# Performance work log

Hardware: AMD Instinct MI355X
Metric: run time of the kernel (lower is better)

## Reference

```python
import jax, jax.numpy as jnp
import numpy as np

QMAX = 127.0
QMIN = -128.0


def setup_inputs() -> dict:
    key = jax.random.key(0)
    k1, k2, k3 = jax.random.split(key, 3)
    B, N, D, O = 4, 4096, 2048, 2048
    x = jax.random.normal(k1, (B, N, D), dtype=jnp.float32)
    weight = jax.random.normal(k2, (O, D), dtype=jnp.float32)
    bias = jax.random.normal(k3, (O,), dtype=jnp.float32)
    return {"x": x, "weight": weight, "bias": bias}


def reference(x, weight, bias):
    # --- per-row symmetric int8 quantization of the weight [O, D] ---
    w_max = jnp.clip(jnp.max(jnp.abs(weight), axis=1, keepdims=True), 1e-8, None)
    w_scale = (w_max / QMAX)                     # [O, 1]
    w_q = jnp.clip(jnp.round(weight / w_scale), QMIN, QMAX).astype(jnp.int8)
    w_scale = w_scale.squeeze(1).astype(jnp.float32)  # [O]

    # --- dynamic per-row symmetric int8 quantization of x [B, N, D] ---
    x_max = jnp.max(jnp.abs(x), axis=2, keepdims=True)       # [B, N, 1]
    x_scale = jnp.maximum(x_max / QMAX, 1e-12)               # [B, N, 1]
    x_q = jnp.clip(jnp.round(x / x_scale), QMIN, QMAX).astype(jnp.int8)

    # --- int8 GEMM accumulated in int32: [B,N,D] x [O,D]^T -> [B,N,O] ---
    acc = jnp.einsum("bnd,od->bno", x_q.astype(jnp.int32), w_q.astype(jnp.int32))

    # --- dequantize with per-row activation scale and per-out-channel weight scale ---
    y = acc.astype(jnp.float32) * x_scale.astype(jnp.float32) * w_scale[None, None, :]
    y = y + bias
    return y.astype(x.dtype)
```

## Files before the change

kernel.cpp:

```cpp
#include <hip/hip_runtime.h>
#include <stdint.h>
#include <stddef.h>

typedef int v4i __attribute__((ext_vector_type(4)));

#define GLOAD_LDS16(g, l) __builtin_amdgcn_global_load_lds( \
    (const __attribute__((address_space(1))) void*)(g),     \
    (__attribute__((address_space(3))) void*)(l), 16, 0, 0)

__device__ __forceinline__ int pack4(float4 f, float s) {
    int a = (int)rintf(f.x / s); a = a < -128 ? -128 : (a > 127 ? 127 : a);
    int b = (int)rintf(f.y / s); b = b < -128 ? -128 : (b > 127 ? 127 : b);
    int c = (int)rintf(f.z / s); c = c < -128 ? -128 : (c > 127 ? 127 : c);
    int d = (int)rintf(f.w / s); d = d < -128 ? -128 : (d > 127 ? 127 : d);
    return (a & 255) | ((b & 255) << 8) | ((c & 255) << 16) | ((d & 255) << 24);
}

__global__ __launch_bounds__(256) void quant_rows_2048(
    const float* __restrict__ in, signed char* __restrict__ q,
    float* __restrict__ scales, float floorv)
{
    const int lane = threadIdx.x & 63;
    const int row  = blockIdx.x * 4 + (threadIdx.x >> 6);
    const float* rp = in + (size_t)row * 2048;

    float4 v[8];
#pragma unroll
    for (int j = 0; j < 2; ++j) {
        const float4* p = (const float4*)(rp + j * 1024 + lane * 16);
#pragma unroll
        for (int i = 0; i < 4; ++i) v[j * 4 + i] = p[i];
    }
    float am = 0.0f;
#pragma unroll
    for (int i = 0; i < 8; ++i) {
        am = fmaxf(am, fabsf(v[i].x));
        am = fmaxf(am, fabsf(v[i].y));
        am = fmaxf(am, fabsf(v[i].z));
        am = fmaxf(am, fabsf(v[i].w));
    }
#pragma unroll
    for (int off = 32; off; off >>= 1) am = fmaxf(am, __shfl_xor(am, off));
    const float s = fmaxf(am / 127.0f, floorv);

#pragma unroll
    for (int j = 0; j < 2; ++j) {
        int4 pk;
        pk.x = pack4(v[j * 4 + 0], s);
        pk.y = pack4(v[j * 4 + 1], s);
        pk.z = pack4(v[j * 4 + 2], s);
        pk.w = pack4(v[j * 4 + 3], s);
        *(int4*)(q + (size_t)row * 2048 + j * 1024 + lane * 16) = pk;
    }
    if (lane == 0) scales[row] = s;
}

__global__ __launch_bounds__(512, 2) void gemm_i8_pipe(
    const signed char* __restrict__ xq, const signed char* __restrict__ wq,
    const float* __restrict__ xs, const float* __restrict__ ws,
    const float* __restrict__ bias, float* __restrict__ out, int K)
{
    __shared__ __align__(16) signed char lds[131072];

    const int tid  = threadIdx.x;
    const int lane = tid & 63;
    const int wid  = tid >> 6;
    const int wm   = wid >> 2;
    const int wn   = wid & 3;

    const int nwg  = gridDim.x * gridDim.y;
    int orig = blockIdx.y * gridDim.x + blockIdx.x;
    int swz  = ((nwg & 7) == 0) ? ((orig & 7) * (nwg >> 3) + (orig >> 3)) : orig;
    const int brow = (swz / gridDim.x) * 256;
    const int bcol = (swz % gridDim.x) * 256;

    const int srow = tid >> 2;
    const int gch  = (((tid & 3) ^ ((tid >> 3) & 3)) << 4);
    const int lofs = tid << 4;
    const signed char* gA = xq + (size_t)(brow + srow) * K;
    const signed char* gB = wq + (size_t)(bcol + srow) * K;

#define ST_A(tt, half) GLOAD_LDS16(gA + (size_t)(half) * 128 * K + (size_t)(tt) * 64 + gch, \
                                   lds + ((((tt) & 3) << 14) + ((half) << 13) + lofs))
#define ST_B(tt, half) GLOAD_LDS16(gB + (size_t)(half) * 128 * K + (size_t)(tt) * 64 + gch, \
                                   lds + (65536 + (((tt) & 3) << 14) + ((half) << 13) + lofs))

    const int rl   = lane & 15;
    const int ko   = lane >> 4;
    const int slot = ((ko ^ ((rl >> 1) & 3)) << 4);

#define FRAG_A(buf, r) (*(const v4i*)(lds + (((buf) << 14) + (r) * 64 + slot)))
#define FRAG_B(buf, r) (*(const v4i*)(lds + (65536 + ((buf) << 14) + (r) * 64 + slot)))

    v4i acc[8][4] = {};

#define MFMA8(M0, M1)                                                              \
    do {                                                                           \
        __builtin_amdgcn_s_setprio(1);                                             \
        acc[M0][0] = __builtin_amdgcn_mfma_i32_16x16x64_i8(a0, bf0, acc[M0][0], 0, 0, 0); \
        acc[M0][1] = __builtin_amdgcn_mfma_i32_16x16x64_i8(a0, bf1, acc[M0][1], 0, 0, 0); \
        acc[M0][2] = __builtin_amdgcn_mfma_i32_16x16x64_i8(a0, bf2, acc[M0][2], 0, 0, 0); \
        acc[M0][3] = __builtin_amdgcn_mfma_i32_16x16x64_i8(a0, bf3, acc[M0][3], 0, 0, 0); \
        acc[M1][0] = __builtin_amdgcn_mfma_i32_16x16x64_i8(a1, bf0, acc[M1][0], 0, 0, 0); \
        acc[M1][1] = __builtin_amdgcn_mfma_i32_16x16x64_i8(a1, bf1, acc[M1][1], 0, 0, 0); \
        acc[M1][2] = __builtin_amdgcn_mfma_i32_16x16x64_i8(a1, bf2, acc[M1][2], 0, 0, 0); \
        acc[M1][3] = __builtin_amdgcn_mfma_i32_16x16x64_i8(a1, bf3, acc[M1][3], 0, 0, 0); \
        __builtin_amdgcn_s_setprio(0);                                             \
    } while (0)

#define BAR()  __builtin_amdgcn_s_barrier()
#define LGKM0() asm volatile("s_waitcnt lgkmcnt(0)" ::: "memory")

    auto tile = [&](int t, bool issue) {
        const int buf = t & 3;
        const int ar  = wm * 128 + rl;
        const int br  = wn * 64 + rl;
        v4i bf0 = FRAG_B(buf, br);
        v4i bf1 = FRAG_B(buf, br + 16);
        v4i bf2 = FRAG_B(buf, br + 32);
        v4i bf3 = FRAG_B(buf, br + 48);
        v4i a0  = FRAG_A(buf, ar);
        v4i a1  = FRAG_A(buf, ar + 16);
        if (issue) ST_A(t + 3, 0);
        BAR(); LGKM0();
        MFMA8(0, 1);
        BAR();
        a0 = FRAG_A(buf, ar + 32);
        a1 = FRAG_A(buf, ar + 48);
        if (issue) ST_A(t + 3, 1);
        BAR(); LGKM0();
        MFMA8(2, 3);
        BAR();
        a0 = FRAG_A(buf, ar + 64);
        a1 = FRAG_A(buf, ar + 80);
        if (issue) ST_B(t + 3, 0);
        BAR(); LGKM0();
        MFMA8(4, 5);
        BAR();
        a0 = FRAG_A(buf, ar + 96);
        a1 = FRAG_A(buf, ar + 112);
        if (issue) ST_B(t + 3, 1);
        BAR(); LGKM0();
        MFMA8(6, 7);
    };

    ST_A(0, 0); ST_A(0, 1); ST_B(0, 0); ST_B(0, 1);
    ST_A(1, 0); ST_A(1, 1); ST_B(1, 0); ST_B(1, 1);
    ST_A(2, 0); ST_A(2, 1); ST_B(2, 0); ST_B(2, 1);
    asm volatile("s_waitcnt vmcnt(8)" ::: "memory");
    BAR();

    const int NT = K >> 6;
    int t = 0;
    for (; t < NT - 3; ++t) {
        tile(t, true);
        asm volatile("s_waitcnt vmcnt(8)" ::: "memory");
        BAR();
    }
    tile(NT - 3, false);
    asm volatile("s_waitcnt vmcnt(4)" ::: "memory");
    BAR();
    tile(NT - 2, false);
    asm volatile("s_waitcnt vmcnt(0)" ::: "memory");
    BAR();
    tile(NT - 1, false);

    const int rg = lane >> 4;
#pragma unroll
    for (int n = 0; n < 4; ++n) {
        const int col = bcol + wn * 64 + n * 16 + rl;
        const float wsc = ws[col];
        const float bv  = bias[col];
#pragma unroll
        for (int m = 0; m < 8; ++m) {
#pragma unroll
            for (int j = 0; j < 4; ++j) {
                const int row = brow + wm * 128 + m * 16 + rg * 4 + j;
                out[(size_t)row * 2048 + col] =
                    (float)acc[m][n][j] * xs[row] * wsc + bv;
            }
        }
    }
#undef ST_A
#undef ST_B
#undef FRAG_A
#undef FRAG_B
#undef MFMA8
#undef BAR
#undef LGKM0
}

extern "C" void kernel_launch(void* const* d_in, const int* in_sizes, int n_in,
                              void* d_out, int out_size, void* d_ws, size_t ws_size,
                              hipStream_t stream) {
    const float* x    = (const float*)d_in[0];
    const float* w    = (const float*)d_in[1];
    const float* bias = (const float*)d_in[2];
    float* out = (float*)d_out;

    const int D = 2048;
    const int O = in_sizes[2];
    const int M = in_sizes[0] / D;

    char* wsb = (char*)d_ws;
    signed char* xq  = (signed char*)wsb;
    signed char* wqp = (signed char*)(wsb + (size_t)M * D);
    float* xs  = (float*)(wsb + (size_t)M * D + (size_t)O * D);
    float* wsc = (float*)(wsb + (size_t)M * D + (size_t)O * D + (size_t)M * 4);

    quant_rows_2048<<<M / 4, 256, 0, stream>>>(x, xq, xs, 1e-12f);
    quant_rows_2048<<<O / 4, 256, 0, stream>>>(w, wqp, wsc, 1e-8f / 127.0f);

    dim3 grid(O / 256, M / 256);
    gemm_i8_pipe<<<grid, 512, 0, stream>>>(xq, wqp, xs, wsc, bias, out, D);
}
```

Measured before the change: 126.0 us.

## Software-pipeline LDS fragment reads one phase ahead of MFMA in GEMM loop

Restructures the main GEMM loop so the A and B LDS fragment reads for the next phase (and the next tile's B fragments) are issued before the current MFMA group. It waits only with lgkmcnt(3) instead of draining all LDS reads, which is meant to hide LDS latency behind matrix-core work. The per-tile lambda and its peeled tail are replaced by a single loop with conditional stores and vmcnt waits. This adds register pressure from the double-buffered fragments and relies on the lgkmcnt counting matching the order in which global-to-LDS loads and LDS reads are issued. A wrong count could read stale data.

```diff
diff --git a/kernel.cpp b/kernel.cpp
--- a/kernel.cpp
+++ b/kernel.cpp
@@ -93,77 +93,74 @@
 #define FRAG_B(buf, r) (*(const v4i*)(lds + (65536 + ((buf) << 14) + (r) * 64 + slot)))
 
     v4i acc[8][4] = {};
+    const int ar = wm * 128 + rl;
+    const int br = wn * 64 + rl;
 
 #define MFMA8(M0, M1)                                                              \
     do {                                                                           \
         __builtin_amdgcn_s_setprio(1);                                             \
-        acc[M0][0] = __builtin_amdgcn_mfma_i32_16x16x64_i8(a0, bf0, acc[M0][0], 0, 0, 0); \
-        acc[M0][1] = __builtin_amdgcn_mfma_i32_16x16x64_i8(a0, bf1, acc[M0][1], 0, 0, 0); \
-        acc[M0][2] = __builtin_amdgcn_mfma_i32_16x16x64_i8(a0, bf2, acc[M0][2], 0, 0, 0); \
-        acc[M0][3] = __builtin_amdgcn_mfma_i32_16x16x64_i8(a0, bf3, acc[M0][3], 0, 0, 0); \
-        acc[M1][0] = __builtin_amdgcn_mfma_i32_16x16x64_i8(a1, bf0, acc[M1][0], 0, 0, 0); \
-        acc[M1][1] = __builtin_amdgcn_mfma_i32_16x16x64_i8(a1, bf1, acc[M1][1], 0, 0, 0); \
-        acc[M1][2] = __builtin_amdgcn_mfma_i32_16x16x64_i8(a1, bf2, acc[M1][2], 0, 0, 0); \
-        acc[M1][3] = __builtin_amdgcn_mfma_i32_16x16x64_i8(a1, bf3, acc[M1][3], 0, 0, 0); \
+        acc[M0][0] = __builtin_amdgcn_mfma_i32_16x16x64_i8(a0, bc0, acc[M0][0], 0, 0, 0); \
+        acc[M0][1] = __builtin_amdgcn_mfma_i32_16x16x64_i8(a0, bc1, acc[M0][1], 0, 0, 0); \
+        acc[M0][2] = __builtin_amdgcn_mfma_i32_16x16x64_i8(a0, bc2, acc[M0][2], 0, 0, 0); \
+        acc[M0][3] = __builtin_amdgcn_mfma_i32_16x16x64_i8(a0, bc3, acc[M0][3], 0, 0, 0); \
+        acc[M1][0] = __builtin_amdgcn_mfma_i32_16x16x64_i8(a1, bc0, acc[M1][0], 0, 0, 0); \
+        acc[M1][1] = __builtin_amdgcn_mfma_i32_16x16x64_i8(a1, bc1, acc[M1][1], 0, 0, 0); \
+        acc[M1][2] = __builtin_amdgcn_mfma_i32_16x16x64_i8(a1, bc2, acc[M1][2], 0, 0, 0); \
+        acc[M1][3] = __builtin_amdgcn_mfma_i32_16x16x64_i8(a1, bc3, acc[M1][3], 0, 0, 0); \
         __builtin_amdgcn_s_setprio(0);                                             \
     } while (0)
 
-#define BAR()  __builtin_amdgcn_s_barrier()
-#define LGKM0() asm volatile("s_waitcnt lgkmcnt(0)" ::: "memory")
-
-    auto tile = [&](int t, bool issue) {
-        const int buf = t & 3;
-        const int ar  = wm * 128 + rl;
-        const int br  = wn * 64 + rl;
-        v4i bf0 = FRAG_B(buf, br);
-        v4i bf1 = FRAG_B(buf, br + 16);
-        v4i bf2 = FRAG_B(buf, br + 32);
-        v4i bf3 = FRAG_B(buf, br + 48);
-        v4i a0  = FRAG_A(buf, ar);
-        v4i a1  = FRAG_A(buf, ar + 16);
-        if (issue) ST_A(t + 3, 0);
-        BAR(); LGKM0();
-        MFMA8(0, 1);
-        BAR();
-        a0 = FRAG_A(buf, ar + 32);
-        a1 = FRAG_A(buf, ar + 48);
-        if (issue) ST_A(t + 3, 1);
-        BAR(); LGKM0();
-        MFMA8(2, 3);
-        BAR();
-        a0 = FRAG_A(buf, ar + 64);
-        a1 = FRAG_A(buf, ar + 80);
-        if (issue) ST_B(t + 3, 0);
-        BAR(); LGKM0();
-        MFMA8(4, 5);
-        BAR();
-        a0 = FRAG_A(buf, ar + 96);
-        a1 = FRAG_A(buf, ar + 112);
-        if (issue) ST_B(t + 3, 1);
-        BAR(); LGKM0();
-        MFMA8(6, 7);
-    };
+#define BAR()   __builtin_amdgcn_s_barrier()
+#define LGKM3() do { asm volatile("s_waitcnt lgkmcnt(3)" ::: "memory"); \
+                     __builtin_amdgcn_sched_barrier(0); } while (0)
 
     ST_A(0, 0); ST_A(0, 1); ST_B(0, 0); ST_B(0, 1);
     ST_A(1, 0); ST_A(1, 1); ST_B(1, 0); ST_B(1, 1);
     ST_A(2, 0); ST_A(2, 1); ST_B(2, 0); ST_B(2, 1);
-    asm volatile("s_waitcnt vmcnt(8)" ::: "memory");
-    BAR();
-
-    const int NT = K >> 6;
-    int t = 0;
-    for (; t < NT - 3; ++t) {
-        tile(t, true);
-        asm volatile("s_waitcnt vmcnt(8)" ::: "memory");
-        BAR();
-    }
-    tile(NT - 3, false);
     asm volatile("s_waitcnt vmcnt(4)" ::: "memory");
     BAR();
-    tile(NT - 2, false);
-    asm volatile("s_waitcnt vmcnt(0)" ::: "memory");
-    BAR();
-    tile(NT - 1, false);
+
+    v4i bc0 = FRAG_B(0, br);
+    v4i bc1 = FRAG_B(0, br + 16);
+    v4i bc2 = FRAG_B(0, br + 32);
+    v4i bc3 = FRAG_B(0, br + 48);
+    v4i a0  = FRAG_A(0, ar);
+    v4i a1  = FRAG_A(0, ar + 16);
+    v4i bn0, bn1, bn2, bn3, na0, na1;
+
+    const int NT = K >> 6;
+    for (int t = 0; t < NT; ++t) {
+        const int buf  = t & 3;
+        const int nbuf = (t + 1) & 3;
+        const bool st  = (t + 3 < NT);
+        na0 = FRAG_A(buf, ar + 32); na1 = FRAG_A(buf, ar + 48); bn0 = FRAG_B(nbuf, br);
+        if (st) ST_A(t + 3, 0);
+        BAR(); LGKM3();
+        MFMA8(0, 1);
+        BAR();
+        a0 = na0; a1 = na1;
+        na0 = FRAG_A(buf, ar + 64); na1 = FRAG_A(buf, ar + 80); bn1 = FRAG_B(nbuf, br + 16);
+        if (st) ST_A(t + 3, 1);
+        BAR(); LGKM3();
+        MFMA8(2, 3);
+        BAR();
+        a0 = na0; a1 = na1;
+        na0 = FRAG_A(buf, ar + 96); na1 = FRAG_A(buf, ar + 112); bn2 = FRAG_B(nbuf, br + 32);
+        if (st) ST_B(t + 3, 0);
+        BAR(); LGKM3();
+        MFMA8(4, 5);
+        BAR();
+        a0 = na0; a1 = na1;
+        na0 = FRAG_A(nbuf, ar); na1 = FRAG_A(nbuf, ar + 16); bn3 = FRAG_B(nbuf, br + 48);
+        if (st) ST_B(t + 3, 1);
+        BAR(); LGKM3();
+        MFMA8(6, 7);
+        if (t + 4 == NT)      asm volatile("s_waitcnt vmcnt(0)" ::: "memory");
+        else if (t + 4 < NT)  asm volatile("s_waitcnt vmcnt(4)" ::: "memory");
+        BAR();
+        a0 = na0; a1 = na1;
+        bc0 = bn0; bc1 = bn1; bc2 = bn2; bc3 = bn3;
+    }
 
     const int rg = lane >> 4;
 #pragma unroll
@@ -187,7 +184,7 @@
 #undef FRAG_B
 #undef MFMA8
 #undef BAR
-#undef LGKM0
+#undef LGKM3
 }
 
 extern "C" void kernel_launch(void* const* d_in, const int* in_sizes, int n_in,
```

After: 135.3 us. 1.07x slower.
